# Performance work log

Measured on AMD Instinct MI355X. Metric: run time of the kernel, lower is better.

## Reference

```python
import jax, jax.numpy as jnp
import numpy as np

GAMMA = 0.98
LBDA = 0.93
EPSI = 0.2
NUM_ACTIONS = 6


def future_returns(rewards, dones, values, gamma):
    # rewards, values: [B, T] float; dones: [B, T] bool
    last = jnp.where(dones[:, -1], rewards[:, -1], values[:, -1])  # Rs[:, T-1]

    def step(carry, xs):
        r_t, d_t = xs
        nv = jnp.where(d_t, jnp.zeros_like(carry), carry)
        R = r_t + gamma * nv
        return R, R

    # time-major inputs for t = 0..T-2, scanned in reverse (t = T-2 .. 0)
    xs = (rewards[:, :-1].T, dones[:, :-1].T)
    _, Rs_head = jax.lax.scan(step, last, xs, reverse=True)  # [T-1, B]
    return jnp.concatenate([Rs_head.T, last[:, None]], axis=1)  # [B, T]


def generalized_advantage(rewards, dones, values, gamma, lbda):
    next_values = jnp.where(dones[:, :-1], 0.0, values[:, 1:])
    td_err = rewards[:, :-1] + gamma * next_values - values[:, :-1]  # [B, T-1]

    def step(gae, xs):
        td_t, d_t = xs
        gae = jnp.where(d_t, jnp.zeros_like(gae), gae)
        gae = td_t + gamma * lbda * gae
        return gae, gae

    xs = (td_err.T, dones[:, :-1].T)
    init = jnp.zeros_like(td_err[:, -1])
    _, A = jax.lax.scan(step, init, xs, reverse=True)  # [T-1, B]
    return A.T  # [B, T-1]


def setup_inputs() -> dict:
    key = jax.random.key(0)
    k1, k2, k3, k4, k5, k6 = jax.random.split(key, 6)
    B, T = 2048, 1024
    rewards = jax.random.normal(k1, (B, T), dtype=jnp.float32)
    values = jax.random.normal(k2, (B, T), dtype=jnp.float32)
    logits = jax.random.normal(k3, (B, T, NUM_ACTIONS), dtype=jnp.float32)
    logits_old = jax.random.normal(k4, (B, T, NUM_ACTIONS), dtype=jnp.float32)
    dones = jax.random.randint(k5, (B, T), 0, 2).astype(jnp.bool_)
    actions = jax.random.randint(k6, (B, T), 0, NUM_ACTIONS, dtype=jnp.int32)
    return {"rewards": rewards, "values": values, "logits": logits,
            "logits_old": logits_old, "dones": dones, "actions": actions}


def reference(rewards, values, logits, logits_old, dones, actions):
    sg = jax.lax.stop_gradient
    log_probs = jax.nn.log_softmax(logits, axis=-1)
    log_probs_old = jax.nn.log_softmax(logits_old, axis=-1)

    V = sg(values)  # values_trainable.detach()
    Rs = sg(future_returns(rewards, dones, V, GAMMA))          # [B, T]
    A = generalized_advantage(rewards, dones, V, GAMMA, LBDA)  # [B, T-1]

    # one-hot einsum == gather of chosen-action log-probs
    log_pis = jnp.take_along_axis(log_probs, actions[..., None], axis=-1)[..., 0]
    log_pis_old = jnp.take_along_axis(log_probs_old, actions[..., None], axis=-1)[..., 0]

    r = jnp.exp(log_pis - sg(log_pis_old))[:, :-1]
    # faithful to torch.clip(min=1-eps, max=eps): min applied then max -> constant eps
    r_clipped = jnp.clip(r, 1.0 - EPSI, EPSI)

    ppo_loss = -jnp.minimum(r * A, r_clipped * A).mean()
    value_loss = jnp.square(sg(Rs) - values).mean()
    entropy_loss = -log_pis.mean()
    return jnp.stack([ppo_loss, value_loss, entropy_loss])  # [3]
```

## Files before the change

kernel.cpp:

```cpp
#include <hip/hip_runtime.h>
#include <math.h>

#define GAMMA 0.98f
#define LBDA  0.93f
#define GL    (GAMMA * LBDA)
constexpr int B  = 2048;
constexpr int T  = 1024;

__device__ __forceinline__ float logpi(float x0, float x1, float x2,
                                       float x3, float x4, float x5, int a) {
    float m = fmaxf(fmaxf(fmaxf(x0, x1), fmaxf(x2, x3)), fmaxf(x4, x5));
    float s = __expf(x0 - m) + __expf(x1 - m) + __expf(x2 - m) +
              __expf(x3 - m) + __expf(x4 - m) + __expf(x5 - m);
    float lse = m + __logf(s);
    float r = x0;
    r = (a == 1) ? x1 : r;
    r = (a == 2) ? x2 : r;
    r = (a == 3) ? x3 : r;
    r = (a == 4) ? x4 : r;
    r = (a == 5) ? x5 : r;
    return r - lse;
}

__global__ __launch_bounds__(512, 1) void k_fused(
        const float2* __restrict__ rw2, const float2* __restrict__ vl2,
        const float*  __restrict__ vl1,
        const int2* __restrict__ dn2, const int2* __restrict__ ac2,
        const float4* __restrict__ lg4, const float4* __restrict__ lgo4,
        float* __restrict__ part_e, float* __restrict__ part_v,
        float* __restrict__ part_p) {
    int j = threadIdx.x;
    int b = blockIdx.x;

    const float4* Lrow = lg4  + (size_t)b * 1536;
    const float4* Orow = lgo4 + (size_t)b * 1536;
    int rbase = b * 512 + j;

    float4 A0 = Lrow[3 * j], A1 = Lrow[3 * j + 1], A2 = Lrow[3 * j + 2];
    float4 B0 = Orow[3 * j], B1 = Orow[3 * j + 1], B2 = Orow[3 * j + 2];
    float2 rw = rw2[rbase], vlv = vl2[rbase];
    int2 dn = dn2[rbase], aa = ac2[rbase];
    int vidx = 2 * j + 2;
    vidx = (vidx > 1022) ? 1022 : vidx;
    float vnext = vl1[(size_t)b * T + vidx];

    float lp0  = logpi(A0.x, A0.y, A0.z, A0.w, A1.x, A1.y, aa.x);
    float lp1  = logpi(A1.z, A1.w, A2.x, A2.y, A2.z, A2.w, aa.y);
    float lpo0 = logpi(B0.x, B0.y, B0.z, B0.w, B1.x, B1.y, aa.x);
    float lpo1 = logpi(B1.z, B1.w, B2.x, B2.y, B2.z, B2.w, aa.y);
    float rr0 = __expf(lp0 - lpo0), rr1 = __expf(lp1 - lpo1);

    __shared__ float wa1[8], wb1[8], wa2[8], wb2[8];
    __shared__ float red[24];

    float rwk[2] = {rw.x, rw.y};
    float vk[3]  = {vlv.x, vlv.y, vnext};
    int   dk[2]  = {dn.x, dn.y};

    float b1[2], c1[2], b2[2], c2[2];
    #pragma unroll
    for (int k = 0; k < 2; ++k) {
        bool d = dk[k] != 0;
        c1[k] = d ? 0.0f : GAMMA;
        b1[k] = rwk[k];
        c2[k] = d ? 0.0f : GL;
        b2[k] = rwk[k] + (d ? 0.0f : GAMMA * vk[k + 1]) - vk[k];
    }
    if (j == 511) {
        b1[1] = dk[1] ? rwk[1] : vk[1];
        c1[1] = 0.0f;
        b2[1] = 0.0f;
        c2[1] = 0.0f;
    }

    float a1 = 1.0f, bb1 = 0.0f, a2 = 1.0f, bb2 = 0.0f;
    #pragma unroll
    for (int k = 1; k >= 0; --k) {
        bb1 = b1[k] + c1[k] * bb1;  a1 = c1[k] * a1;
        bb2 = b2[k] + c2[k] * bb2;  a2 = c2[k] * a2;
    }

    int lane = j & 63, wv = j >> 6;
    #pragma unroll
    for (int d = 1; d < 64; d <<= 1) {
        float an1 = __shfl_down(a1, d), bn1 = __shfl_down(bb1, d);
        float an2 = __shfl_down(a2, d), bn2 = __shfl_down(bb2, d);
        if (lane + d < 64) {
            bb1 = a1 * bn1 + bb1;  a1 = a1 * an1;
            bb2 = a2 * bn2 + bb2;  a2 = a2 * an2;
        }
    }
    if (lane == 0) { wa1[wv] = a1; wb1[wv] = bb1; wa2[wv] = a2; wb2[wv] = bb2; }
    float a1s = __shfl_down(a1, 1), b1s = __shfl_down(bb1, 1);
    float a2s = __shfl_down(a2, 1), b2s = __shfl_down(bb2, 1);
    __syncthreads();

    float x1 = 0.0f, x2 = 0.0f;
    for (int w2 = 7; w2 > wv; --w2) {
        x1 = wa1[w2] * x1 + wb1[w2];
        x2 = wa2[w2] * x2 + wb2[w2];
    }
    float cin1 = (lane == 63) ? x1 : (a1s * x1 + b1s);
    float cin2 = (lane == 63) ? x2 : (a2s * x2 + b2s);

    float rrk[2] = {rr0, rr1};
    float vsum = 0.0f, psum = 0.0f;
    float R = cin1, A = cin2;
    #pragma unroll
    for (int k = 1; k >= 0; --k) {
        R = b1[k] + c1[k] * R;
        float dv = R - vk[k];
        vsum += dv * dv;
        A = b2[k] + c2[k] * A;
        if (2 * j + k < T - 1) {
            psum += fminf(rrk[k] * A, 0.2f * A);
        }
    }
    float es = lp0 + lp1;

    #pragma unroll
    for (int d = 32; d; d >>= 1) {
        es   += __shfl_xor(es, d);
        vsum += __shfl_xor(vsum, d);
        psum += __shfl_xor(psum, d);
    }
    if (lane == 0) { red[wv] = es; red[8 + wv] = vsum; red[16 + wv] = psum; }
    __syncthreads();
    if (j == 0) {
        float te = 0.0f, tv = 0.0f, tp = 0.0f;
        #pragma unroll
        for (int w2 = 0; w2 < 8; ++w2) {
            te += red[w2]; tv += red[8 + w2]; tp += red[16 + w2];
        }
        part_e[b] = te;
        part_v[b] = tv;
        part_p[b] = tp;
    }
}

__global__ __launch_bounds__(256) void k_fin(
        const float* __restrict__ part_e, const float* __restrict__ part_v,
        const float* __restrict__ part_p, float* __restrict__ out) {
    int tid = threadIdx.x;
    float e = 0.0f, v = 0.0f, p = 0.0f;
    for (int i = tid; i < B; i += 256) {
        e += part_e[i];
        v += part_v[i];
        p += part_p[i];
    }
    #pragma unroll
    for (int d = 32; d; d >>= 1) {
        e += __shfl_xor(e, d);
        v += __shfl_xor(v, d);
        p += __shfl_xor(p, d);
    }
    __shared__ float sm[12];
    int lane = tid & 63, wv = tid >> 6;
    if (lane == 0) { sm[wv] = e; sm[4 + wv] = v; sm[8 + wv] = p; }
    __syncthreads();
    if (tid == 0) {
        float te = sm[0] + sm[1] + sm[2] + sm[3];
        float tv = sm[4] + sm[5] + sm[6] + sm[7];
        float tp = sm[8] + sm[9] + sm[10] + sm[11];
        out[0] = -tp / (float)(B * (T - 1));
        out[1] =  tv / (float)(B * T);
        out[2] = -te / (float)(B * T);
    }
}

extern "C" void kernel_launch(void* const* d_in, const int* in_sizes, int n_in,
                              void* d_out, int out_size, void* d_ws, size_t ws_size,
                              hipStream_t stream) {
    const float* rewards    = (const float*)d_in[0];
    const float* values     = (const float*)d_in[1];
    const float* logits     = (const float*)d_in[2];
    const float* logits_old = (const float*)d_in[3];
    const int*   dones      = (const int*)d_in[4];
    const int*   actions    = (const int*)d_in[5];

    float* part_e = (float*)d_ws;
    float* part_v = part_e + B;
    float* part_p = part_v + B;

    k_fused<<<B, 512, 0, stream>>>(
        (const float2*)rewards, (const float2*)values, values,
        (const int2*)dones, (const int2*)actions,
        (const float4*)logits, (const float4*)logits_old,
        part_e, part_v, part_p);

    k_fin<<<1, 256, 0, stream>>>(part_e, part_v, part_p, (float*)d_out);
}
```

Before: 159.0 us.

## Process each row with one wavefront, sixteen timesteps per thread

Each block now holds a single 64-thread wavefront that handles a full row. Each thread loads 16 consecutive timesteps with float4/int4 loads, runs the two reverse scans serially in registers, and then does a wave-level shuffle scan. This removes the cross-wave shared-memory scan, both __syncthreads, and the block-level reduction. In exchange there are fewer threads per block, and logits are read with strided per-thread float4 loads that coalesce less well, so memory parallelism may drop.

```diff
diff --git a/kernel.cpp b/kernel.cpp
--- a/kernel.cpp
+++ b/kernel.cpp
@@ -22,10 +22,10 @@
     return r - lse;
 }
 
-__global__ __launch_bounds__(512, 1) void k_fused(
-        const float2* __restrict__ rw2, const float2* __restrict__ vl2,
+__global__ __launch_bounds__(64, 4) void k_fused(
+        const float4* __restrict__ rw4, const float4* __restrict__ vl4,
         const float*  __restrict__ vl1,
-        const int2* __restrict__ dn2, const int2* __restrict__ ac2,
+        const int4* __restrict__ dn4, const int4* __restrict__ ac4,
         const float4* __restrict__ lg4, const float4* __restrict__ lgo4,
         float* __restrict__ part_e, float* __restrict__ part_v,
         float* __restrict__ part_p) {
@@ -34,89 +34,108 @@
 
     const float4* Lrow = lg4  + (size_t)b * 1536;
     const float4* Orow = lgo4 + (size_t)b * 1536;
-    int rbase = b * 512 + j;
-
-    float4 A0 = Lrow[3 * j], A1 = Lrow[3 * j + 1], A2 = Lrow[3 * j + 2];
-    float4 B0 = Orow[3 * j], B1 = Orow[3 * j + 1], B2 = Orow[3 * j + 2];
-    float2 rw = rw2[rbase], vlv = vl2[rbase];
-    int2 dn = dn2[rbase], aa = ac2[rbase];
-    int vidx = 2 * j + 2;
-    vidx = (vidx > 1022) ? 1022 : vidx;
-    float vnext = vl1[(size_t)b * T + vidx];
-
-    float lp0  = logpi(A0.x, A0.y, A0.z, A0.w, A1.x, A1.y, aa.x);
-    float lp1  = logpi(A1.z, A1.w, A2.x, A2.y, A2.z, A2.w, aa.y);
-    float lpo0 = logpi(B0.x, B0.y, B0.z, B0.w, B1.x, B1.y, aa.x);
-    float lpo1 = logpi(B1.z, B1.w, B2.x, B2.y, B2.z, B2.w, aa.y);
-    float rr0 = __expf(lp0 - lpo0), rr1 = __expf(lp1 - lpo1);
-
-    __shared__ float wa1[8], wb1[8], wa2[8], wb2[8];
-    __shared__ float red[24];
-
-    float rwk[2] = {rw.x, rw.y};
-    float vk[3]  = {vlv.x, vlv.y, vnext};
-    int   dk[2]  = {dn.x, dn.y};
-
-    float b1[2], c1[2], b2[2], c2[2];
-    #pragma unroll
-    for (int k = 0; k < 2; ++k) {
-        bool d = dk[k] != 0;
-        c1[k] = d ? 0.0f : GAMMA;
-        b1[k] = rwk[k];
-        c2[k] = d ? 0.0f : GL;
-        b2[k] = rwk[k] + (d ? 0.0f : GAMMA * vk[k + 1]) - vk[k];
-    }
-    if (j == 511) {
-        b1[1] = dk[1] ? rwk[1] : vk[1];
-        c1[1] = 0.0f;
-        b2[1] = 0.0f;
-        c2[1] = 0.0f;
+    const float4* rwr  = rw4  + (size_t)b * 256;
+    const float4* vlr  = vl4  + (size_t)b * 256;
+    const int4*   dnr  = dn4  + (size_t)b * 256;
+    const int4*   acr  = ac4  + (size_t)b * 256;
+
+    float rw[16], v[17], r[16];
+    #pragma unroll
+    for (int c = 0; c < 4; ++c) {
+        float4 t0 = rwr[4 * j + c];
+        float4 t1 = vlr[4 * j + c];
+        rw[4 * c + 0] = t0.x; rw[4 * c + 1] = t0.y;
+        rw[4 * c + 2] = t0.z; rw[4 * c + 3] = t0.w;
+        v[4 * c + 0] = t1.x; v[4 * c + 1] = t1.y;
+        v[4 * c + 2] = t1.z; v[4 * c + 3] = t1.w;
+    }
+    int nidx = 16 * j + 16;
+    nidx = (nidx > 1023) ? 1023 : nidx;
+    v[16] = vl1[(size_t)b * 1024 + nidx];
+
+    float es = 0.0f;
+    unsigned dbits = 0;
+    #pragma unroll
+    for (int c = 0; c < 4; ++c) {
+        int base = 24 * j + 6 * c;
+        float4 A0 = Lrow[base],     A1 = Lrow[base + 1], A2 = Lrow[base + 2];
+        float4 A3 = Lrow[base + 3], A4 = Lrow[base + 4], A5 = Lrow[base + 5];
+        float4 B0 = Orow[base],     B1 = Orow[base + 1], B2 = Orow[base + 2];
+        float4 B3 = Orow[base + 3], B4 = Orow[base + 4], B5 = Orow[base + 5];
+        int4 ac = acr[4 * j + c];
+        int4 dn = dnr[4 * j + c];
+
+        float lp0 = logpi(A0.x, A0.y, A0.z, A0.w, A1.x, A1.y, ac.x);
+        float lq0 = logpi(B0.x, B0.y, B0.z, B0.w, B1.x, B1.y, ac.x);
+        float lp1 = logpi(A1.z, A1.w, A2.x, A2.y, A2.z, A2.w, ac.y);
+        float lq1 = logpi(B1.z, B1.w, B2.x, B2.y, B2.z, B2.w, ac.y);
+        float lp2 = logpi(A3.x, A3.y, A3.z, A3.w, A4.x, A4.y, ac.z);
+        float lq2 = logpi(B3.x, B3.y, B3.z, B3.w, B4.x, B4.y, ac.z);
+        float lp3 = logpi(A4.z, A4.w, A5.x, A5.y, A5.z, A5.w, ac.w);
+        float lq3 = logpi(B4.z, B4.w, B5.x, B5.y, B5.z, B5.w, ac.w);
+
+        r[4 * c + 0] = __expf(lp0 - lq0);
+        r[4 * c + 1] = __expf(lp1 - lq1);
+        r[4 * c + 2] = __expf(lp2 - lq2);
+        r[4 * c + 3] = __expf(lp3 - lq3);
+        es += lp0 + lp1 + lp2 + lp3;
+
+        dbits |= (dn.x != 0 ? 1u : 0u) << (4 * c + 0);
+        dbits |= (dn.y != 0 ? 1u : 0u) << (4 * c + 1);
+        dbits |= (dn.z != 0 ? 1u : 0u) << (4 * c + 2);
+        dbits |= (dn.w != 0 ? 1u : 0u) << (4 * c + 3);
     }
 
     float a1 = 1.0f, bb1 = 0.0f, a2 = 1.0f, bb2 = 0.0f;
     #pragma unroll
-    for (int k = 1; k >= 0; --k) {
-        bb1 = b1[k] + c1[k] * bb1;  a1 = c1[k] * a1;
-        bb2 = b2[k] + c2[k] * bb2;  a2 = c2[k] * a2;
-    }
-
-    int lane = j & 63, wv = j >> 6;
+    for (int k = 15; k >= 0; --k) {
+        bool d = (dbits >> k) & 1u;
+        float c1 = d ? 0.0f : GAMMA;
+        float b1 = rw[k];
+        float c2 = d ? 0.0f : GL;
+        float b2 = rw[k] + (d ? 0.0f : GAMMA * v[k + 1]) - v[k];
+        if (j == 63 && k == 15) {
+            b1 = d ? rw[15] : v[15];
+            c1 = 0.0f; b2 = 0.0f; c2 = 0.0f;
+        }
+        bb1 = b1 + c1 * bb1;  a1 = c1 * a1;
+        bb2 = b2 + c2 * bb2;  a2 = c2 * a2;
+    }
+
     #pragma unroll
     for (int d = 1; d < 64; d <<= 1) {
         float an1 = __shfl_down(a1, d), bn1 = __shfl_down(bb1, d);
         float an2 = __shfl_down(a2, d), bn2 = __shfl_down(bb2, d);
-        if (lane + d < 64) {
+        if (j + d < 64) {
             bb1 = a1 * bn1 + bb1;  a1 = a1 * an1;
             bb2 = a2 * bn2 + bb2;  a2 = a2 * an2;
         }
     }
-    if (lane == 0) { wa1[wv] = a1; wb1[wv] = bb1; wa2[wv] = a2; wb2[wv] = bb2; }
-    float a1s = __shfl_down(a1, 1), b1s = __shfl_down(bb1, 1);
-    float a2s = __shfl_down(a2, 1), b2s = __shfl_down(bb2, 1);
-    __syncthreads();
-
-    float x1 = 0.0f, x2 = 0.0f;
-    for (int w2 = 7; w2 > wv; --w2) {
-        x1 = wa1[w2] * x1 + wb1[w2];
-        x2 = wa2[w2] * x2 + wb2[w2];
-    }
-    float cin1 = (lane == 63) ? x1 : (a1s * x1 + b1s);
-    float cin2 = (lane == 63) ? x2 : (a2s * x2 + b2s);
-
-    float rrk[2] = {rr0, rr1};
+    float b1s = __shfl_down(bb1, 1), b2s = __shfl_down(bb2, 1);
+    float cin1 = (j == 63) ? 0.0f : b1s;
+    float cin2 = (j == 63) ? 0.0f : b2s;
+
     float vsum = 0.0f, psum = 0.0f;
     float R = cin1, A = cin2;
     #pragma unroll
-    for (int k = 1; k >= 0; --k) {
-        R = b1[k] + c1[k] * R;
-        float dv = R - vk[k];
+    for (int k = 15; k >= 0; --k) {
+        bool d = (dbits >> k) & 1u;
+        float c1 = d ? 0.0f : GAMMA;
+        float b1 = rw[k];
+        float c2 = d ? 0.0f : GL;
+        float b2 = rw[k] + (d ? 0.0f : GAMMA * v[k + 1]) - v[k];
+        if (j == 63 && k == 15) {
+            b1 = d ? rw[15] : v[15];
+            c1 = 0.0f; b2 = 0.0f; c2 = 0.0f;
+        }
+        R = b1 + c1 * R;
+        float dv = R - v[k];
         vsum += dv * dv;
-        A = b2[k] + c2[k] * A;
-        if (2 * j + k < T - 1) {
-            psum += fminf(rrk[k] * A, 0.2f * A);
-        }
-    }
-    float es = lp0 + lp1;
+        A = b2 + c2 * A;
+        if (16 * j + k < T - 1) {
+            psum += fminf(r[k] * A, 0.2f * A);
+        }
+    }
 
     #pragma unroll
     for (int d = 32; d; d >>= 1) {
@@ -124,17 +143,10 @@
         vsum += __shfl_xor(vsum, d);
         psum += __shfl_xor(psum, d);
     }
-    if (lane == 0) { red[wv] = es; red[8 + wv] = vsum; red[16 + wv] = psum; }
-    __syncthreads();
     if (j == 0) {
-        float te = 0.0f, tv = 0.0f, tp = 0.0f;
-        #pragma unroll
-        for (int w2 = 0; w2 < 8; ++w2) {
-            te += red[w2]; tv += red[8 + w2]; tp += red[16 + w2];
-        }
-        part_e[b] = te;
-        part_v[b] = tv;
-        part_p[b] = tp;
+        part_e[b] = es;
+        part_v[b] = vsum;
+        part_p[b] = psum;
     }
 }
 
@@ -182,9 +194,9 @@
     float* part_v = part_e + B;
     float* part_p = part_v + B;
 
-    k_fused<<<B, 512, 0, stream>>>(
-        (const float2*)rewards, (const float2*)values, values,
-        (const int2*)dones, (const int2*)actions,
+    k_fused<<<B, 64, 0, stream>>>(
+        (const float4*)rewards, (const float4*)values, values,
+        (const int4*)dones, (const int4*)actions,
         (const float4*)logits, (const float4*)logits_old,
         part_e, part_v, part_p);
 
```

Measured after the change: 211.8 us. 1.33x slower.
